# Kernel optimization log

Measured on AMD Instinct MI355X. Metric: run time of the kernel, lower is better.

Reference implementation:

```python
import jax, jax.numpy as jnp
import numpy as np

EPS = 1e-8

def _cos(a, b):
    # a: [B,1,d], b: [B,C,d] -> [B,C]  (torch.nn.CosineSimilarity(dim=2) semantics, eps=1e-8)
    na = jnp.maximum(jnp.sqrt(jnp.sum(a * a, axis=-1)), EPS)
    nb = jnp.maximum(jnp.sqrt(jnp.sum(b * b, axis=-1)), EPS)
    return jnp.sum(a * b, axis=-1) / (na * nb)

def setup_inputs() -> dict:
    key = jax.random.key(0)
    ks = jax.random.split(key, 20)
    B, C = 2048, 64
    BERT, CTRY, CODE, MIX = 768, 24, 8, 24
    N_CODES, N_COUNTRIES, GAZ = 654, 250, 9
    s = 0.02
    inp = {
        "placename_tensor": jax.random.normal(ks[0], (B, BERT), jnp.float32),
        "other_locs_tensor": jax.random.normal(ks[1], (B, BERT), jnp.float32),
        "doc_tensor": jax.random.normal(ks[2], (B, BERT), jnp.float32),
        "feature_codes": jax.random.randint(ks[3], (B, C), 0, N_CODES, jnp.int64 if jax.config.jax_enable_x64 else jnp.int32),
        "country_codes": jax.random.randint(ks[4], (B, C), 0, N_COUNTRIES, jnp.int64 if jax.config.jax_enable_x64 else jnp.int32),
        "gaz_info": jax.random.normal(ks[5], (B, C, GAZ), jnp.float32),
        # learned params
        "code_emb_table": jax.random.normal(ks[6], (N_CODES, CODE), jnp.float32),
        "country_emb_table": jax.random.normal(ks[7], (N_COUNTRIES, BERT), jnp.float32),
        "W_cet": jax.random.normal(ks[8], (CTRY, BERT), jnp.float32) * s,
        "b_cet": jnp.zeros((CTRY,), jnp.float32),
        "W_t2c": jax.random.normal(ks[9], (CTRY, BERT), jnp.float32) * s,
        "b_t2c": jnp.zeros((CTRY,), jnp.float32),
        "W_ctx": jax.random.normal(ks[10], (CTRY, BERT), jnp.float32) * s,
        "b_ctx": jnp.zeros((CTRY,), jnp.float32),
        "W_code": jax.random.normal(ks[11], (CODE, BERT), jnp.float32) * s,
        "b_code": jnp.zeros((CODE,), jnp.float32),
        "W_mix1": jax.random.normal(ks[12], (MIX, 13), jnp.float32) * 0.2,
        "b_mix1": jnp.zeros((MIX,), jnp.float32),
        "W_mix2": jax.random.normal(ks[13], (MIX, MIX), jnp.float32) * 0.2,
        "b_mix2": jnp.zeros((MIX,), jnp.float32),
        "W_last": jax.random.normal(ks[14], (1, MIX), jnp.float32) * 0.2,
        "b_last": jnp.zeros((1,), jnp.float32),
    }
    return inp

def reference(placename_tensor, other_locs_tensor, doc_tensor, feature_codes, country_codes,
              gaz_info, code_emb_table, country_emb_table, W_cet, b_cet, W_t2c, b_t2c,
              W_ctx, b_ctx, W_code, b_code, W_mix1, b_mix1, W_mix2, b_mix2, W_last, b_last):
    # eval mode: dropout = identity
    x = placename_tensor @ W_t2c.T + b_t2c            # [B,24]
    x_code = placename_tensor @ W_code.T + b_code     # [B,8]
    x_other = other_locs_tensor @ W_ctx.T + b_ctx     # [B,24]
    x_doc = doc_tensor @ W_ctx.T + b_ctx              # [B,24]
    fc = code_emb_table[feature_codes]                # [B,C,8]
    cc = country_emb_table[country_codes] @ W_cet.T + b_cet  # [B,C,24]
    sim_country = _cos(x[:, None, :], cc)             # [B,C]
    sim_code = _cos(x_code[:, None, :], fc)
    sim_other = _cos(x_other[:, None, :], cc)
    sim_doc = _cos(x_doc[:, None, :], cc)
    both = jnp.concatenate([sim_country[..., None], sim_code[..., None],
                            sim_other[..., None], sim_doc[..., None], gaz_info], axis=2)  # [B,C,13]
    h = jax.nn.sigmoid(both @ W_mix1.T + b_mix1)
    h = jax.nn.sigmoid(h @ W_mix2.T + b_mix2)
    last = jnp.squeeze(h @ W_last.T + b_last, axis=2)  # [B,C]
    return jax.nn.softmax(last, axis=1)
```

## Files before the change

kernel.cpp:

```cpp
#include <hip/hip_runtime.h>
#include <math.h>

#define BB 2048
#define CC 64
#define BERT 768
#define N_CTRY 250
#define N_CODES 654

#define OFF_PCHAT   0
#define OFF_CODEHAT (250*24)
#define OFF_XALL    (OFF_CODEHAT + 654*8)
#define OFF_SSQ     (OFF_XALL + 2048*80)

#define RPB 8
#define ROWGRPS (BB / RPB)
#define PROJ_BLOCKS (5 * ROWGRPS)

__global__ __launch_bounds__(256) void k_proj(
    const float* __restrict__ place, const float* __restrict__ other,
    const float* __restrict__ doc,
    const float* __restrict__ W_t2c, const float* __restrict__ b_t2c,
    const float* __restrict__ W_code, const float* __restrict__ b_code,
    const float* __restrict__ W_ctx, const float* __restrict__ b_ctx,
    const float* __restrict__ ctab, const float* __restrict__ W_cet,
    const float* __restrict__ b_cet, const float* __restrict__ code_emb,
    float* __restrict__ ws) {
  __shared__ float s_ss[RPB][4];
  __shared__ float s_p24[24];
  __shared__ float s_inv1;

  const int bid = blockIdx.x;
  const int tid = threadIdx.x;
  const int w = tid >> 6, lane = tid & 63;

  if (bid < PROJ_BLOCKS) {
    float* xall = ws + OFF_XALL;
    float* ssq  = ws + OFF_SSQ;
    const int cb = bid / ROWGRPS;
    const int rg = bid % ROWGRPS;
    const int row0 = rg * RPB;
    const int j0 = cb * 16 + w * 4;
    const float* wbase; const float* xbase; const float* bbase; int jb;
    if (j0 < 24)      { wbase = W_t2c;  bbase = b_t2c;  jb = j0;      xbase = place; }
    else if (j0 < 32) { wbase = W_code; bbase = b_code; jb = j0 - 24; xbase = place; }
    else if (j0 < 56) { wbase = W_ctx;  bbase = b_ctx;  jb = j0 - 32; xbase = other; }
    else              { wbase = W_ctx;  bbase = b_ctx;  jb = j0 - 56; xbase = doc;   }
    const int jsub = lane & 3, kq = lane >> 2;
    const float bias = bbase[jb + jsub];

    float4 wv[12];
    {
      const float4* wr = (const float4*)(wbase + (size_t)(jb + jsub) * BERT);
#pragma unroll
      for (int i = 0; i < 12; ++i) wv[i] = wr[kq + 16 * i];
    }

    for (int r = 0; r < RPB; ++r) {
      const int row = row0 + r;
      const float4* xr = (const float4*)(xbase + (size_t)row * BERT);
      float s0 = 0.f, s1 = 0.f, s2 = 0.f, s3 = 0.f;
#pragma unroll
      for (int i = 0; i < 12; i += 4) {
        float4 a0 = xr[kq + 16 * (i + 0)];
        float4 a1 = xr[kq + 16 * (i + 1)];
        float4 a2 = xr[kq + 16 * (i + 2)];
        float4 a3 = xr[kq + 16 * (i + 3)];
        s0 += a0.x * wv[i+0].x + a0.y * wv[i+0].y + a0.z * wv[i+0].z + a0.w * wv[i+0].w;
        s1 += a1.x * wv[i+1].x + a1.y * wv[i+1].y + a1.z * wv[i+1].z + a1.w * wv[i+1].w;
        s2 += a2.x * wv[i+2].x + a2.y * wv[i+2].y + a2.z * wv[i+2].z + a2.w * wv[i+2].w;
        s3 += a3.x * wv[i+3].x + a3.y * wv[i+3].y + a3.z * wv[i+3].z + a3.w * wv[i+3].w;
      }
      float acc = (s0 + s1) + (s2 + s3);
#pragma unroll
      for (int m = 4; m <= 32; m <<= 1) acc += __shfl_xor(acc, m, 64);
      const float val = acc + bias;
      if (kq == 0) xall[(size_t)row * 80 + j0 + jsub] = val;
      float v2 = val * val;
      v2 += __shfl_xor(v2, 1, 64);
      v2 += __shfl_xor(v2, 2, 64);
      if (lane == 0) s_ss[r][w] = v2;
    }
    __syncthreads();
    if (tid < RPB * 2) {
      const int r = tid >> 1, s = tid & 1;
      ssq[(size_t)(row0 + r) * 10 + cb * 2 + s] = s_ss[r][2 * s] + s_ss[r][2 * s + 1];
    }
  } else if (bid < PROJ_BLOCKS + N_CTRY) {
    float* pchat = ws + OFF_PCHAT;
    const int b = bid - PROJ_BLOCKS;
    float4 xa[3];
#pragma unroll
    for (int i = 0; i < 3; ++i)
      xa[i] = ((const float4*)(ctab + (size_t)b * BERT))[lane + 64 * i];
    float acc6[6];
#pragma unroll
    for (int jj = 0; jj < 6; ++jj) acc6[jj] = 0.f;
#pragma unroll
    for (int jj = 0; jj < 6; ++jj) {
      const int j = w * 6 + jj;
      const float4* wr = (const float4*)(W_cet + (size_t)j * BERT);
#pragma unroll
      for (int i = 0; i < 3; ++i) {
        float4 wv = wr[lane + 64 * i];
        acc6[jj] += xa[i].x * wv.x + xa[i].y * wv.y + xa[i].z * wv.z + xa[i].w * wv.w;
      }
    }
#pragma unroll
    for (int s = 32; s >= 1; s >>= 1)
#pragma unroll
      for (int jj = 0; jj < 6; ++jj) acc6[jj] += __shfl_xor(acc6[jj], s, 64);
    if (lane == 0) {
#pragma unroll
      for (int jj = 0; jj < 6; ++jj) s_p24[w * 6 + jj] = acc6[jj] + b_cet[w * 6 + jj];
    }
    __syncthreads();
    if (tid == 0) {
      float ss = 0.f;
      for (int k = 0; k < 24; ++k) ss += s_p24[k] * s_p24[k];
      s_inv1 = 1.f / fmaxf(sqrtf(ss), 1e-8f);
    }
    __syncthreads();
    if (tid < 24) pchat[b * 24 + tid] = s_p24[tid] * s_inv1;
  } else {
    float* codehat = ws + OFF_CODEHAT;
    const int idx = (bid - PROJ_BLOCKS - N_CTRY) * 256 + tid;
    if (idx < N_CODES) {
      float v[8];
      float ss = 0.f;
#pragma unroll
      for (int k = 0; k < 8; ++k) { v[k] = code_emb[idx * 8 + k]; ss += v[k] * v[k]; }
      const float inv = 1.f / fmaxf(sqrtf(ss), 1e-8f);
#pragma unroll
      for (int k = 0; k < 8; ++k) codehat[idx * 8 + k] = v[k] * inv;
    }
  }
}

__global__ __launch_bounds__(128) void k_classify(
    const int* __restrict__ fcodes, const int* __restrict__ ccodes,
    const float* __restrict__ gaz,
    const float* __restrict__ W_mix1, const float* __restrict__ b_mix1,
    const float* __restrict__ W_mix2, const float* __restrict__ b_mix2,
    const float* __restrict__ W_last, const float* __restrict__ b_last,
    const float* __restrict__ ws, float* __restrict__ out) {
  __shared__ float s_pch[N_CTRY * 25];
  __shared__ float s_gz[2 * CC * 9];
  const int tid = threadIdx.x;
  const int w = tid >> 6, lane = tid & 63;
  const int row0 = blockIdx.x * 2;

  {
    const float* pch = ws + OFF_PCHAT;
    for (int e = tid; e < N_CTRY * 24; e += 128)
      s_pch[(e / 24) * 25 + (e % 24)] = pch[e];
    float4* gz4 = (float4*)s_gz;
    const float4* g4 = (const float4*)(gaz + (size_t)row0 * CC * 9);
    for (int e = tid; e < 2 * CC * 9 / 4; e += 128) gz4[e] = g4[e];
  }
  __syncthreads();

  const int row = __builtin_amdgcn_readfirstlane(row0 + w);
  const float* xv = ws + OFF_XALL + (size_t)row * 80;
  const float* q  = ws + OFF_SSQ + (size_t)row * 10;
  const float g0 = q[0] + q[1] + q[2];
  const float g1 = q[3];
  const float g2 = q[4] + q[5] + q[6];
  const float g3 = q[7] + q[8] + q[9];
  const float inv0 = 1.f / fmaxf(sqrtf(g0), 1e-8f);
  const float inv1 = 1.f / fmaxf(sqrtf(g1), 1e-8f);
  const float inv2 = 1.f / fmaxf(sqrtf(g2), 1e-8f);
  const float inv3 = 1.f / fmaxf(sqrtf(g3), 1e-8f);

  const int cidx = ccodes[row * CC + lane];
  const int fidx = fcodes[row * CC + lane];

  float cc[24];
#pragma unroll
  for (int k = 0; k < 24; ++k) cc[k] = s_pch[cidx * 25 + k];
  float cd[8];
  {
    const float4* q4 = (const float4*)(ws + OFF_CODEHAT + fidx * 8);
#pragma unroll
    for (int i = 0; i < 2; ++i) {
      float4 v = q4[i];
      cd[4*i+0] = v.x; cd[4*i+1] = v.y; cd[4*i+2] = v.z; cd[4*i+3] = v.w;
    }
  }

  float sc = 0.f, so = 0.f, sd = 0.f, sq = 0.f;
#pragma unroll
  for (int k = 0; k < 24; ++k) {
    const float ck = cc[k];
    sc += xv[k] * ck;
    so += xv[32 + k] * ck;
    sd += xv[56 + k] * ck;
  }
#pragma unroll
  for (int k = 0; k < 8; ++k) sq += xv[24 + k] * cd[k];

  float f[13];
  f[0] = sc * inv0;
  f[1] = sq * inv1;
  f[2] = so * inv2;
  f[3] = sd * inv3;
#pragma unroll
  for (int i = 0; i < 9; ++i) f[4 + i] = s_gz[(w * CC + lane) * 9 + i];

  float h1[24];
#pragma unroll
  for (int j = 0; j < 24; ++j) {
    float a = b_mix1[j];
#pragma unroll
    for (int i = 0; i < 13; ++i) a += W_mix1[j * 13 + i] * f[i];
    h1[j] = 1.f / (1.f + __expf(-a));
  }
  float h2[24];
#pragma unroll
  for (int j = 0; j < 24; ++j) {
    float a = b_mix2[j];
#pragma unroll
    for (int i = 0; i < 24; ++i) a += W_mix2[j * 24 + i] * h1[i];
    h2[j] = 1.f / (1.f + __expf(-a));
  }
  float last = b_last[0];
#pragma unroll
  for (int k = 0; k < 24; ++k) last += W_last[k] * h2[k];

  float mx = last;
#pragma unroll
  for (int s = 32; s >= 1; s >>= 1) mx = fmaxf(mx, __shfl_xor(mx, s, 64));
  const float e = __expf(last - mx);
  float ssum = e;
#pragma unroll
  for (int s = 32; s >= 1; s >>= 1) ssum += __shfl_xor(ssum, s, 64);
  out[row * CC + lane] = e / ssum;
}

extern "C" void kernel_launch(void* const* d_in, const int* in_sizes, int n_in,
                              void* d_out, int out_size, void* d_ws, size_t ws_size,
                              hipStream_t stream) {
  const float* place   = (const float*)d_in[0];
  const float* other   = (const float*)d_in[1];
  const float* doc     = (const float*)d_in[2];
  const int*   fcodes  = (const int*)d_in[3];
  const int*   ccodes  = (const int*)d_in[4];
  const float* gaz     = (const float*)d_in[5];
  const float* code_emb= (const float*)d_in[6];
  const float* ctab    = (const float*)d_in[7];
  const float* W_cet   = (const float*)d_in[8];
  const float* b_cet   = (const float*)d_in[9];
  const float* W_t2c   = (const float*)d_in[10];
  const float* b_t2c   = (const float*)d_in[11];
  const float* W_ctx   = (const float*)d_in[12];
  const float* b_ctx   = (const float*)d_in[13];
  const float* W_code  = (const float*)d_in[14];
  const float* b_code  = (const float*)d_in[15];
  const float* W_mix1  = (const float*)d_in[16];
  const float* b_mix1  = (const float*)d_in[17];
  const float* W_mix2  = (const float*)d_in[18];
  const float* b_mix2  = (const float*)d_in[19];
  const float* W_last  = (const float*)d_in[20];
  const float* b_last  = (const float*)d_in[21];
  float* ws  = (float*)d_ws;
  float* out = (float*)d_out;

  k_proj<<<PROJ_BLOCKS + N_CTRY + 3, 256, 0, stream>>>(
      place, other, doc, W_t2c, b_t2c, W_code, b_code, W_ctx, b_ctx,
      ctab, W_cet, b_cet, code_emb, ws);
  k_classify<<<BB / 2, 128, 0, stream>>>(fcodes, ccodes, gaz, W_mix1, b_mix1,
                                         W_mix2, b_mix2, W_last, b_last, ws, out);
}
```

Before: 148.1 us.

## Batch projection shuffles and process four rows per classify block

In k_proj, the per-row dot-product partials for all 8 rows are kept in registers and reduced together with interleaved cross-lane shuffles, instead of reducing each row serially. k_classify now handles 4 rows per 256-thread block rather than 2 per 128-thread block. That halves how often the ~24 KB country table is staged into shared memory. The gaz features are read straight from global memory with float4 loads instead of going through a shared-memory staging buffer. Those float4 loads sit at 36-byte strides, so they are not 16-byte aligned and depend on the hardware tolerating unaligned vector loads.

```diff
diff --git a/kernel.cpp b/kernel.cpp
--- a/kernel.cpp
+++ b/kernel.cpp
@@ -55,9 +55,10 @@
       for (int i = 0; i < 12; ++i) wv[i] = wr[kq + 16 * i];
     }
 
+    float acc[RPB];
+#pragma unroll
     for (int r = 0; r < RPB; ++r) {
-      const int row = row0 + r;
-      const float4* xr = (const float4*)(xbase + (size_t)row * BERT);
+      const float4* xr = (const float4*)(xbase + (size_t)(row0 + r) * BERT);
       float s0 = 0.f, s1 = 0.f, s2 = 0.f, s3 = 0.f;
 #pragma unroll
       for (int i = 0; i < 12; i += 4) {
@@ -70,15 +71,28 @@
         s2 += a2.x * wv[i+2].x + a2.y * wv[i+2].y + a2.z * wv[i+2].z + a2.w * wv[i+2].w;
         s3 += a3.x * wv[i+3].x + a3.y * wv[i+3].y + a3.z * wv[i+3].z + a3.w * wv[i+3].w;
       }
-      float acc = (s0 + s1) + (s2 + s3);
-#pragma unroll
-      for (int m = 4; m <= 32; m <<= 1) acc += __shfl_xor(acc, m, 64);
-      const float val = acc + bias;
-      if (kq == 0) xall[(size_t)row * 80 + j0 + jsub] = val;
-      float v2 = val * val;
-      v2 += __shfl_xor(v2, 1, 64);
-      v2 += __shfl_xor(v2, 2, 64);
-      if (lane == 0) s_ss[r][w] = v2;
+      acc[r] = (s0 + s1) + (s2 + s3);
+    }
+
+#pragma unroll
+    for (int m = 4; m <= 32; m <<= 1)
+#pragma unroll
+      for (int r = 0; r < RPB; ++r) acc[r] += __shfl_xor(acc[r], m, 64);
+
+    float v2[RPB];
+#pragma unroll
+    for (int r = 0; r < RPB; ++r) {
+      const float val = acc[r] + bias;
+      if (kq == 0) xall[(size_t)(row0 + r) * 80 + j0 + jsub] = val;
+      v2[r] = val * val;
+    }
+#pragma unroll
+    for (int r = 0; r < RPB; ++r) v2[r] += __shfl_xor(v2[r], 1, 64);
+#pragma unroll
+    for (int r = 0; r < RPB; ++r) v2[r] += __shfl_xor(v2[r], 2, 64);
+    if (lane == 0) {
+#pragma unroll
+      for (int r = 0; r < RPB; ++r) s_ss[r][w] = v2[r];
     }
     __syncthreads();
     if (tid < RPB * 2) {
@@ -101,8 +115,8 @@
       const float4* wr = (const float4*)(W_cet + (size_t)j * BERT);
 #pragma unroll
       for (int i = 0; i < 3; ++i) {
-        float4 wv = wr[lane + 64 * i];
-        acc6[jj] += xa[i].x * wv.x + xa[i].y * wv.y + xa[i].z * wv.z + xa[i].w * wv.w;
+        float4 wvv = wr[lane + 64 * i];
+        acc6[jj] += xa[i].x * wvv.x + xa[i].y * wvv.y + xa[i].z * wvv.z + xa[i].w * wvv.w;
       }
     }
 #pragma unroll
@@ -136,7 +150,7 @@
   }
 }
 
-__global__ __launch_bounds__(128) void k_classify(
+__global__ __launch_bounds__(256) void k_classify(
     const int* __restrict__ fcodes, const int* __restrict__ ccodes,
     const float* __restrict__ gaz,
     const float* __restrict__ W_mix1, const float* __restrict__ b_mix1,
@@ -144,18 +158,14 @@
     const float* __restrict__ W_last, const float* __restrict__ b_last,
     const float* __restrict__ ws, float* __restrict__ out) {
   __shared__ float s_pch[N_CTRY * 25];
-  __shared__ float s_gz[2 * CC * 9];
   const int tid = threadIdx.x;
   const int w = tid >> 6, lane = tid & 63;
-  const int row0 = blockIdx.x * 2;
+  const int row0 = blockIdx.x * 4;
 
   {
     const float* pch = ws + OFF_PCHAT;
-    for (int e = tid; e < N_CTRY * 24; e += 128)
+    for (int e = tid; e < N_CTRY * 24; e += 256)
       s_pch[(e / 24) * 25 + (e % 24)] = pch[e];
-    float4* gz4 = (float4*)s_gz;
-    const float4* g4 = (const float4*)(gaz + (size_t)row0 * CC * 9);
-    for (int e = tid; e < 2 * CC * 9 / 4; e += 128) gz4[e] = g4[e];
   }
   __syncthreads();
 
@@ -203,8 +213,14 @@
   f[1] = sq * inv1;
   f[2] = so * inv2;
   f[3] = sd * inv3;
-#pragma unroll
-  for (int i = 0; i < 9; ++i) f[4 + i] = s_gz[(w * CC + lane) * 9 + i];
+  {
+    const float* g = gaz + (size_t)(row * CC + lane) * 9;
+    float4 ga = ((const float4*)g)[0];
+    float4 gb = ((const float4*)g)[1];
+    f[4] = ga.x; f[5] = ga.y; f[6] = ga.z; f[7] = ga.w;
+    f[8] = gb.x; f[9] = gb.y; f[10] = gb.z; f[11] = gb.w;
+    f[12] = g[8];
+  }
 
   float h1[24];
 #pragma unroll
@@ -267,6 +283,6 @@
   k_proj<<<PROJ_BLOCKS + N_CTRY + 3, 256, 0, stream>>>(
       place, other, doc, W_t2c, b_t2c, W_code, b_code, W_ctx, b_ctx,
       ctab, W_cet, b_cet, code_emb, ws);
-  k_classify<<<BB / 2, 128, 0, stream>>>(fcodes, ccodes, gaz, W_mix1, b_mix1,
+  k_classify<<<BB / 4, 256, 0, stream>>>(fcodes, ccodes, gaz, W_mix1, b_mix1,
                                          W_mix2, b_mix2, W_last, b_last, ws, out);
 }
```

New measurement: 143.4 us. 1.03x faster.
